# Performance work log

Hardware: AMD Instinct MI355X
Metric: run time of the kernel (lower is better)

The kernel has to match this reference:

```python
import jax, jax.numpy as jnp
import numpy as np

B, C, D, H, W = 4, 128, 16, 16, 16
CQ = C // 8

def setup_inputs() -> dict:
    key = jax.random.key(0)
    ks = jax.random.split(key, 8)
    s = 0.05
    return {
        "x": jax.random.normal(ks[0], (B, C, D, H, W), dtype=jnp.float32),
        "wq": jax.random.normal(ks[1], (CQ, C), dtype=jnp.float32) * s,
        "bq": jax.random.normal(ks[2], (CQ,), dtype=jnp.float32) * s,
        "wk": jax.random.normal(ks[3], (CQ, C), dtype=jnp.float32) * s,
        "bk": jax.random.normal(ks[4], (CQ,), dtype=jnp.float32) * s,
        "wv": jax.random.normal(ks[5], (C, C), dtype=jnp.float32) * s,
        "bv": jax.random.normal(ks[6], (C,), dtype=jnp.float32) * s,
        "gamma": jax.random.normal(ks[7], (1,), dtype=jnp.float32),
    }

def reference(x, wq, bq, wk, bk, wv, bv, gamma):
    b, c, d, h, w = x.shape
    n = d * h * w
    xf = x.reshape(b, c, n)                                  # [B,C,N]
    # 1x1x1 convs == channel-wise linear projections
    q = jnp.einsum('bcn,qc->bqn', xf, wq) + bq[None, :, None]  # [B,CQ,N]
    k = jnp.einsum('bcn,qc->bqn', xf, wk) + bk[None, :, None]  # [B,CQ,N]
    v = jnp.einsum('bcn,oc->bon', xf, wv) + bv[None, :, None]  # [B,C,N]
    # energy[b,i,j] = sum_c q[b,c,i] * k[b,c,j]  (query permuted to [B,N,CQ])
    energy = jnp.einsum('bci,bcj->bij', q, k)                # [B,N,N]
    attn = jax.nn.softmax(energy, axis=-1)                   # [B,N,N]
    # out = bmm(value, attn^T): out[b,c,i] = sum_j v[b,c,j] * attn[b,i,j]
    out = jnp.einsum('bcj,bij->bci', v, attn)                # [B,C,N]
    out = out.reshape(b, c, d, h, w)
    return gamma[0] * out + x
```

## Files before the change

### kernel.cpp

```cpp
#include <hip/hip_runtime.h>
#include <stdint.h>

#define NT 4096
#define L2E 1.44269504f

typedef short s16x8 __attribute__((ext_vector_type(8)));
typedef short s16x4 __attribute__((ext_vector_type(4)));
typedef float f32x16 __attribute__((ext_vector_type(16)));
typedef float f32x4 __attribute__((ext_vector_type(4)));

__device__ __forceinline__ unsigned short f2bf(float f) {
  unsigned int u = __float_as_uint(f);
  u = u + 0x7FFFu + ((u >> 16) & 1u);
  return (unsigned short)(u >> 16);
}

__device__ __forceinline__ void pack_pa(const float* p, s16x8* pa) {
  unsigned w8[8];
#pragma unroll
  for (int m = 0; m < 8; ++m)
    asm("v_cvt_pk_bf16_f32 %0, %1, %2" : "=v"(w8[m]) : "v"(p[2 * m]), "v"(p[2 * m + 1]));
  unsigned a0 = w8[0], b0 = w8[2]; asm("v_permlane32_swap_b32 %0, %1" : "+v"(a0), "+v"(b0));
  unsigned a1 = w8[1], b1 = w8[3]; asm("v_permlane32_swap_b32 %0, %1" : "+v"(a1), "+v"(b1));
  unsigned c0 = w8[4], d0 = w8[6]; asm("v_permlane32_swap_b32 %0, %1" : "+v"(c0), "+v"(d0));
  unsigned c1 = w8[5], d1 = w8[7]; asm("v_permlane32_swap_b32 %0, %1" : "+v"(c1), "+v"(d1));
  union PW { unsigned u[4]; s16x8 v; } q0, q1;
  q0.u[0] = a0; q0.u[1] = a1; q0.u[2] = b0; q0.u[3] = b1;
  q1.u[0] = c0; q1.u[1] = c1; q1.u[2] = d0; q1.u[3] = d1;
  pa[0] = q0.v; pa[1] = q1.v;
}

__device__ __forceinline__ void merge_write(float* scr, const f32x16 (&acc)[2][4],
                                            int lc, int hi) {
#pragma unroll
  for (int isub = 0; isub < 2; ++isub)
#pragma unroll
    for (int cb = 0; cb < 4; ++cb)
#pragma unroll
      for (int r = 0; r < 16; ++r) {
        int i = isub * 32 + (r & 3) + 8 * (r >> 2) + 4 * hi;
        scr[i * 132 + cb * 32 + lc] = acc[isub][cb][r];
      }
}
__device__ __forceinline__ void merge_add(const float* scr, f32x16 (&acc)[2][4],
                                          int lc, int hi) {
#pragma unroll
  for (int isub = 0; isub < 2; ++isub)
#pragma unroll
    for (int cb = 0; cb < 4; ++cb)
#pragma unroll
      for (int r = 0; r < 16; ++r) {
        int i = isub * 32 + (r & 3) + 8 * (r >> 2) + 4 * hi;
        acc[isub][cb][r] += scr[i * 132 + cb * 32 + lc];
      }
}

__global__ __launch_bounds__(512, 2) void proj_kern(
    const float* __restrict__ x,
    const float* __restrict__ wq, const float* __restrict__ bq,
    const float* __restrict__ wk, const float* __restrict__ bk,
    const float* __restrict__ wv, const float* __restrict__ bv,
    short* __restrict__ qws, short* __restrict__ kws, short* __restrict__ vfrag) {
  __shared__ __align__(16) unsigned short w_s[160 * 128];
  __shared__ __align__(16) unsigned short xv_s[128 * 72];

  int t = threadIdx.x;
  int blk = blockIdx.x;
  int b = blk >> 6;
  int n0 = (blk & 63) * 64;

  for (int i4 = t; i4 < 5120; i4 += 512) {
    int row = i4 >> 5, ka = (i4 & 31) * 4;
    f32x4 v;
    float sc = 1.0f;
    if (row < 128)      v = *(const f32x4*)(wv + row * 128 + ka);
    else if (row < 144) v = *(const f32x4*)(wq + (row - 128) * 128 + ka);
    else              { v = *(const f32x4*)(wk + (row - 144) * 128 + ka); sc = L2E; }
    s16x4 o;
#pragma unroll
    for (int j = 0; j < 4; ++j) o[j] = (short)f2bf(v[j] * sc);
    unsigned byt = ((unsigned)(ka * 2)) ^ (((unsigned)row & 7u) << 4);
    *(s16x4*)((char*)w_s + row * 256 + byt) = o;
  }
  {
    int cL = t >> 4, nn4 = (t & 15) * 4;
    for (int cc = 0; cc < 128; cc += 32) {
      int c = cc + cL;
      f32x4 v = *(const f32x4*)(x + ((size_t)b * 128 + c) * NT + n0 + nn4);
      s16x4 o;
#pragma unroll
      for (int j = 0; j < 4; ++j) o[j] = (short)f2bf(v[j]);
      *(s16x4*)(xv_s + c * 64 + nn4) = o;
    }
  }
  __syncthreads();

  int w = t >> 6, lane = t & 63, lc = lane & 31, hi = lane >> 5;
  int rblk = w >> 1, nc = w & 1;
  int nn = nc * 32 + lc;

  f32x16 zf = {0.f,0.f,0.f,0.f,0.f,0.f,0.f,0.f,0.f,0.f,0.f,0.f,0.f,0.f,0.f,0.f};
  f32x16 acc = zf, acc2 = zf;

#pragma unroll
  for (int kk = 0; kk < 8; ++kk) {
    int kb0 = kk * 16 + hi * 8;
    s16x8 xf;
#pragma unroll
    for (int e = 0; e < 8; ++e) xf[e] = (short)xv_s[(kb0 + e) * 64 + nn];
    unsigned byt = ((unsigned)(kk * 32 + hi * 16)) ^ (((unsigned)lc & 7u) << 4);
    s16x8 af = *(const s16x8*)((const char*)w_s + (rblk * 32 + lc) * 256 + byt);
    acc = __builtin_amdgcn_mfma_f32_32x32x16_bf16(af, xf, acc, 0, 0, 0);
    if (rblk == 3) {
      s16x8 af2 = *(const s16x8*)((const char*)w_s + (128 + lc) * 256 + byt);
      acc2 = __builtin_amdgcn_mfma_f32_32x32x16_bf16(af2, xf, acc2, 0, 0, 0);
    }
  }

  if (rblk == 3) {
    size_t nidx = ((size_t)b * NT + n0 + nn) * 16;
    s16x4 q0, q1, k0, k1;
#pragma unroll
    for (int j = 0; j < 4; ++j) {
      q0[j] = (short)f2bf(acc2[j]      + bq[j + 4 * hi]);
      q1[j] = (short)f2bf(acc2[j + 4]  + bq[j + 8 + 4 * hi]);
      k0[j] = (short)f2bf(acc2[j + 8]  + bk[j + 4 * hi] * L2E);
      k1[j] = (short)f2bf(acc2[j + 12] + bk[j + 8 + 4 * hi] * L2E);
    }
    *(s16x4*)(qws + nidx + 4 * hi)     = q0;
    *(s16x4*)(qws + nidx + 8 + 4 * hi) = q1;
    *(s16x4*)(kws + nidx + 4 * hi)     = k0;
    *(s16x4*)(kws + nidx + 8 + 4 * hi) = k1;
  }

  __syncthreads();
#pragma unroll
  for (int r = 0; r < 16; ++r) {
    int c = rblk * 32 + (r & 3) + 8 * (r >> 2) + 4 * hi;
    xv_s[c * 72 + nn] = f2bf(acc[r] + bv[c]);
  }
  __syncthreads();
#pragma unroll
  for (int p = 0; p < 2; ++p) {
    int gid = t + p * 512;
    int c = gid & 127, ng = gid >> 7;
    s16x8 v = *(const s16x8*)(xv_s + c * 72 + ng * 8);
    size_t idx = (((size_t)b * 256 + (n0 >> 4) + (ng >> 1)) * 128 + c) * 16 + (ng & 1) * 8;
    *(s16x8*)(vfrag + idx) = v;
  }
}

__global__ __launch_bounds__(512, 2) void attn_mfma(
    const short* __restrict__ qws, const short* __restrict__ kws, const short* __restrict__ vfrag,
    const float* __restrict__ x, const float* __restrict__ gp, float* __restrict__ out) {
  __shared__ __align__(16) unsigned char lds[69888];

  int g = blockIdx.x;
  int gg = (g & 7) * 32 + (g >> 3);
  int b = gg >> 6;
  int it = gg & 63;
  int t = threadIdx.x;
  int w = t >> 6, lane = t & 63, lc = lane & 31, hi = lane >> 5;
  int jt0 = w * 512;

  const short* qb = qws + (size_t)b * NT * 16;
  const short* kb = kws + (size_t)b * NT * 16;
  const short* vfb = vfrag + (size_t)b * 256 * 128 * 16;

  s16x8 qf0 = *(const s16x8*)(qb + (size_t)(it * 64 + lc) * 16 + hi * 8);
  s16x8 qf1 = *(const s16x8*)(qb + (size_t)(it * 64 + 32 + lc) * 16 + hi * 8);

  f32x16 zf = {0.f,0.f,0.f,0.f,0.f,0.f,0.f,0.f,0.f,0.f,0.f,0.f,0.f,0.f,0.f,0.f};
  f32x16 acc[2][4];
#pragma unroll
  for (int i = 0; i < 2; ++i)
#pragma unroll
    for (int j = 0; j < 4; ++j) acc[i][j] = zf;
  float lsum0 = 0.f, lsum1 = 0.f;

  s16x8 kf = *(const s16x8*)(kb + (size_t)(jt0 + lc) * 16 + hi * 8);

  for (int st = 0; st < 16; ++st) {
    int jtb = (jt0 >> 4) + st * 2;
    s16x8 vB[2][4];
#pragma unroll
    for (int sl = 0; sl < 2; ++sl)
#pragma unroll
      for (int cb = 0; cb < 4; ++cb)
        vB[sl][cb] = *(const s16x8*)(vfb + ((size_t)(jtb + sl) * 128 + cb * 32 + lc) * 16 + hi * 8);
    s16x8 kn = kf;
    if (st < 15)
      kn = *(const s16x8*)(kb + (size_t)(jt0 + (st + 1) * 32 + lc) * 16 + hi * 8);

    f32x16 e0 = __builtin_amdgcn_mfma_f32_32x32x16_bf16(kf, qf0, zf, 0, 0, 0);
    f32x16 e1 = __builtin_amdgcn_mfma_f32_32x32x16_bf16(kf, qf1, zf, 0, 0, 0);

    float p0[16], p1[16];
#pragma unroll
    for (int r = 0; r < 16; ++r) { p0[r] = __builtin_amdgcn_exp2f(e0[r]); p1[r] = __builtin_amdgcn_exp2f(e1[r]); }
    float a0 = 0.f, a1 = 0.f;
#pragma unroll
    for (int r = 0; r < 16; ++r) { a0 += p0[r]; a1 += p1[r]; }
    lsum0 += a0; lsum1 += a1;

    s16x8 pa0[2], pa1[2];
    pack_pa(p0, pa0);
    pack_pa(p1, pa1);

#pragma unroll
    for (int sl = 0; sl < 2; ++sl)
#pragma unroll
      for (int cb = 0; cb < 4; ++cb) {
        acc[0][cb] = __builtin_amdgcn_mfma_f32_32x32x16_bf16(pa0[sl], vB[sl][cb], acc[0][cb], 0, 0, 0);
        acc[1][cb] = __builtin_amdgcn_mfma_f32_32x32x16_bf16(pa1[sl], vB[sl][cb], acc[1][cb], 0, 0, 0);
      }
    kf = kn;
  }

  float* rg0  = (float*)lds;
  float* rg1  = (float*)(lds + 33792);
  float* lsc  = (float*)(lds + 67584);
  float* linv = (float*)(lds + 69632);

  float lf0 = lsum0 + __shfl_xor(lsum0, 32);
  float lf1 = lsum1 + __shfl_xor(lsum1, 32);
  if (hi == 0) { lsc[w * 64 + lc] = lf0; lsc[w * 64 + 32 + lc] = lf1; }
  __syncthreads();
  if (t < 64) {
    float L = 0.f;
#pragma unroll
    for (int w2 = 0; w2 < 8; ++w2) L += lsc[w2 * 64 + t];
    linv[t] = 1.0f / L;
  }
  if (w == 4) merge_write(rg0, acc, lc, hi);
  if (w == 5) merge_write(rg1, acc, lc, hi);
  __syncthreads();
  if (w == 0) merge_add(rg0, acc, lc, hi);
  if (w == 1) merge_add(rg1, acc, lc, hi);
  __syncthreads();
  if (w == 6) merge_write(rg0, acc, lc, hi);
  if (w == 7) merge_write(rg1, acc, lc, hi);
  __syncthreads();
  if (w == 2) merge_add(rg0, acc, lc, hi);
  if (w == 3) merge_add(rg1, acc, lc, hi);
  __syncthreads();
  if (w == 2) merge_write(rg0, acc, lc, hi);
  if (w == 3) merge_write(rg1, acc, lc, hi);
  __syncthreads();
  if (w == 0) merge_add(rg0, acc, lc, hi);
  if (w == 1) merge_add(rg1, acc, lc, hi);
  __syncthreads();
  if (w == 1) merge_write(rg0, acc, lc, hi);
  __syncthreads();
  if (w == 0) {
    merge_add(rg0, acc, lc, hi);
    merge_write(rg0, acc, lc, hi);
  }
  __syncthreads();

  float gam = gp[0];
  int cc = t >> 2, iq = t & 3;
  const float* xb = x + ((size_t)b * 128 + cc) * NT + it * 64 + iq * 16;
  float* ob = out + ((size_t)b * 128 + cc) * NT + it * 64 + iq * 16;
#pragma unroll
  for (int q2 = 0; q2 < 4; ++q2) {
    f32x4 xv = *(const f32x4*)(xb + q2 * 4);
    f32x4 ov;
#pragma unroll
    for (int j = 0; j < 4; ++j) {
      int i = iq * 16 + q2 * 4 + j;
      ov[j] = gam * rg0[i * 132 + cc] * linv[i] + xv[j];
    }
    *(f32x4*)(ob + q2 * 4) = ov;
  }
}

extern "C" void kernel_launch(void* const* d_in, const int* in_sizes, int n_in,
                              void* d_out, int out_size, void* d_ws, size_t ws_size,
                              hipStream_t stream) {
  const float* x     = (const float*)d_in[0];
  const float* wq    = (const float*)d_in[1];
  const float* bq    = (const float*)d_in[2];
  const float* wk    = (const float*)d_in[3];
  const float* bk    = (const float*)d_in[4];
  const float* wv    = (const float*)d_in[5];
  const float* bv    = (const float*)d_in[6];
  const float* gamma = (const float*)d_in[7];
  float* out = (float*)d_out;

  short* qws   = (short*)d_ws;
  short* kws   = qws + (size_t)4 * NT * 16;
  short* vfrag = kws + (size_t)4 * NT * 16;

  proj_kern<<<256, 512, 0, stream>>>(x, wq, bq, wk, bk, wv, bv, qws, kws, vfrag);
  attn_mfma<<<256, 512, 0, stream>>>(qws, kws, vfrag, x, gamma, out);
}
```

Baseline: 43.54 us.

## Shrink attention tile to 32 queries over 4 waves with 512 blocks

The attention kernel now handles 32 query rows per block with 4 waves of 256 threads, each wave covering 1024 keys, and launches 512 blocks instead of 256 blocks of 512 threads. The smaller accumulator set and LDS footprint are meant to raise occupancy and shorten the cross-wave merge. V loads are split into two halves interleaved with MFMA groups wrapped in setprio. The cost is that each K/V fragment is reused by only one query tile, which doubles K/V traffic relative to the amount of compute.

```diff
diff --git a/kernel.cpp b/kernel.cpp
--- a/kernel.cpp
+++ b/kernel.cpp
@@ -30,29 +30,25 @@
   pa[0] = q0.v; pa[1] = q1.v;
 }
 
-__device__ __forceinline__ void merge_write(float* scr, const f32x16 (&acc)[2][4],
+__device__ __forceinline__ void merge_write(float* scr, const f32x16 (&acc)[4],
                                             int lc, int hi) {
 #pragma unroll
-  for (int isub = 0; isub < 2; ++isub)
-#pragma unroll
-    for (int cb = 0; cb < 4; ++cb)
-#pragma unroll
-      for (int r = 0; r < 16; ++r) {
-        int i = isub * 32 + (r & 3) + 8 * (r >> 2) + 4 * hi;
-        scr[i * 132 + cb * 32 + lc] = acc[isub][cb][r];
-      }
-}
-__device__ __forceinline__ void merge_add(const float* scr, f32x16 (&acc)[2][4],
+  for (int cb = 0; cb < 4; ++cb)
+#pragma unroll
+    for (int r = 0; r < 16; ++r) {
+      int i = (r & 3) + 8 * (r >> 2) + 4 * hi;
+      scr[i * 132 + cb * 32 + lc] = acc[cb][r];
+    }
+}
+__device__ __forceinline__ void merge_add(const float* scr, f32x16 (&acc)[4],
                                           int lc, int hi) {
 #pragma unroll
-  for (int isub = 0; isub < 2; ++isub)
-#pragma unroll
-    for (int cb = 0; cb < 4; ++cb)
-#pragma unroll
-      for (int r = 0; r < 16; ++r) {
-        int i = isub * 32 + (r & 3) + 8 * (r >> 2) + 4 * hi;
-        acc[isub][cb][r] += scr[i * 132 + cb * 32 + lc];
-      }
+  for (int cb = 0; cb < 4; ++cb)
+#pragma unroll
+    for (int r = 0; r < 16; ++r) {
+      int i = (r & 3) + 8 * (r >> 2) + 4 * hi;
+      acc[cb][r] += scr[i * 132 + cb * 32 + lc];
+    }
 }
 
 __global__ __launch_bounds__(512, 2) void proj_kern(
@@ -150,103 +146,83 @@
   }
 }
 
-__global__ __launch_bounds__(512, 2) void attn_mfma(
+__global__ __launch_bounds__(256, 4) void attn_mfma(
     const short* __restrict__ qws, const short* __restrict__ kws, const short* __restrict__ vfrag,
     const float* __restrict__ x, const float* __restrict__ gp, float* __restrict__ out) {
-  __shared__ __align__(16) unsigned char lds[69888];
+  __shared__ __align__(16) unsigned char lds[34432];
 
   int g = blockIdx.x;
-  int gg = (g & 7) * 32 + (g >> 3);
-  int b = gg >> 6;
-  int it = gg & 63;
+  int gg = (g & 7) * 64 + (g >> 3);
+  int b = gg >> 7;
+  int it = gg & 127;
   int t = threadIdx.x;
   int w = t >> 6, lane = t & 63, lc = lane & 31, hi = lane >> 5;
-  int jt0 = w * 512;
+  int jt0 = w * 1024;
 
   const short* qb = qws + (size_t)b * NT * 16;
   const short* kb = kws + (size_t)b * NT * 16;
   const short* vfb = vfrag + (size_t)b * 256 * 128 * 16;
 
-  s16x8 qf0 = *(const s16x8*)(qb + (size_t)(it * 64 + lc) * 16 + hi * 8);
-  s16x8 qf1 = *(const s16x8*)(qb + (size_t)(it * 64 + 32 + lc) * 16 + hi * 8);
+  s16x8 qf = *(const s16x8*)(qb + (size_t)(it * 32 + lc) * 16 + hi * 8);
 
   f32x16 zf = {0.f,0.f,0.f,0.f,0.f,0.f,0.f,0.f,0.f,0.f,0.f,0.f,0.f,0.f,0.f,0.f};
-  f32x16 acc[2][4];
-#pragma unroll
-  for (int i = 0; i < 2; ++i)
-#pragma unroll
-    for (int j = 0; j < 4; ++j) acc[i][j] = zf;
-  float lsum0 = 0.f, lsum1 = 0.f;
-
-  s16x8 kf = *(const s16x8*)(kb + (size_t)(jt0 + lc) * 16 + hi * 8);
-
-  for (int st = 0; st < 16; ++st) {
-    int jtb = (jt0 >> 4) + st * 2;
-    s16x8 vB[2][4];
-#pragma unroll
-    for (int sl = 0; sl < 2; ++sl)
-#pragma unroll
-      for (int cb = 0; cb < 4; ++cb)
-        vB[sl][cb] = *(const s16x8*)(vfb + ((size_t)(jtb + sl) * 128 + cb * 32 + lc) * 16 + hi * 8);
-    s16x8 kn = kf;
-    if (st < 15)
-      kn = *(const s16x8*)(kb + (size_t)(jt0 + (st + 1) * 32 + lc) * 16 + hi * 8);
-
-    f32x16 e0 = __builtin_amdgcn_mfma_f32_32x32x16_bf16(kf, qf0, zf, 0, 0, 0);
-    f32x16 e1 = __builtin_amdgcn_mfma_f32_32x32x16_bf16(kf, qf1, zf, 0, 0, 0);
-
-    float p0[16], p1[16];
-#pragma unroll
-    for (int r = 0; r < 16; ++r) { p0[r] = __builtin_amdgcn_exp2f(e0[r]); p1[r] = __builtin_amdgcn_exp2f(e1[r]); }
-    float a0 = 0.f, a1 = 0.f;
-#pragma unroll
-    for (int r = 0; r < 16; ++r) { a0 += p0[r]; a1 += p1[r]; }
-    lsum0 += a0; lsum1 += a1;
-
-    s16x8 pa0[2], pa1[2];
-    pack_pa(p0, pa0);
-    pack_pa(p1, pa1);
-
-#pragma unroll
-    for (int sl = 0; sl < 2; ++sl)
-#pragma unroll
-      for (int cb = 0; cb < 4; ++cb) {
-        acc[0][cb] = __builtin_amdgcn_mfma_f32_32x32x16_bf16(pa0[sl], vB[sl][cb], acc[0][cb], 0, 0, 0);
-        acc[1][cb] = __builtin_amdgcn_mfma_f32_32x32x16_bf16(pa1[sl], vB[sl][cb], acc[1][cb], 0, 0, 0);
-      }
-    kf = kn;
+  f32x16 acc[4];
+#pragma unroll
+  for (int j = 0; j < 4; ++j) acc[j] = zf;
+  float lsum = 0.f;
+
+  for (int st = 0; st < 32; ++st) {
+    int j0 = jt0 + st * 32;
+    int jtb = j0 >> 4;
+    s16x8 kf = *(const s16x8*)(kb + (size_t)(j0 + lc) * 16 + hi * 8);
+    s16x8 v0[4];
+#pragma unroll
+    for (int cb = 0; cb < 4; ++cb)
+      v0[cb] = *(const s16x8*)(vfb + ((size_t)jtb * 128 + cb * 32 + lc) * 16 + hi * 8);
+
+    f32x16 e = __builtin_amdgcn_mfma_f32_32x32x16_bf16(kf, qf, zf, 0, 0, 0);
+#pragma unroll
+    for (int r = 0; r < 16; ++r) e[r] = __builtin_amdgcn_exp2f(e[r]);
+    float a0 = 0.f;
+#pragma unroll
+    for (int r = 0; r < 16; ++r) a0 += e[r];
+    lsum += a0;
+
+    s16x8 pa[2];
+    pack_pa((const float*)&e, pa);
+
+    __builtin_amdgcn_s_setprio(1);
+#pragma unroll
+    for (int cb = 0; cb < 4; ++cb)
+      acc[cb] = __builtin_amdgcn_mfma_f32_32x32x16_bf16(pa[0], v0[cb], acc[cb], 0, 0, 0);
+    __builtin_amdgcn_s_setprio(0);
+
+    s16x8 v1[4];
+#pragma unroll
+    for (int cb = 0; cb < 4; ++cb)
+      v1[cb] = *(const s16x8*)(vfb + ((size_t)(jtb + 1) * 128 + cb * 32 + lc) * 16 + hi * 8);
+
+    __builtin_amdgcn_s_setprio(1);
+#pragma unroll
+    for (int cb = 0; cb < 4; ++cb)
+      acc[cb] = __builtin_amdgcn_mfma_f32_32x32x16_bf16(pa[1], v1[cb], acc[cb], 0, 0, 0);
+    __builtin_amdgcn_s_setprio(0);
   }
 
   float* rg0  = (float*)lds;
-  float* rg1  = (float*)(lds + 33792);
-  float* lsc  = (float*)(lds + 67584);
-  float* linv = (float*)(lds + 69632);
-
-  float lf0 = lsum0 + __shfl_xor(lsum0, 32);
-  float lf1 = lsum1 + __shfl_xor(lsum1, 32);
-  if (hi == 0) { lsc[w * 64 + lc] = lf0; lsc[w * 64 + 32 + lc] = lf1; }
-  __syncthreads();
-  if (t < 64) {
-    float L = 0.f;
-#pragma unroll
-    for (int w2 = 0; w2 < 8; ++w2) L += lsc[w2 * 64 + t];
-    linv[t] = 1.0f / L;
-  }
-  if (w == 4) merge_write(rg0, acc, lc, hi);
-  if (w == 5) merge_write(rg1, acc, lc, hi);
-  __syncthreads();
-  if (w == 0) merge_add(rg0, acc, lc, hi);
-  if (w == 1) merge_add(rg1, acc, lc, hi);
-  __syncthreads();
-  if (w == 6) merge_write(rg0, acc, lc, hi);
-  if (w == 7) merge_write(rg1, acc, lc, hi);
-  __syncthreads();
-  if (w == 2) merge_add(rg0, acc, lc, hi);
-  if (w == 3) merge_add(rg1, acc, lc, hi);
-  __syncthreads();
+  float* rg1  = (float*)(lds + 16896);
+  float* lsc  = (float*)(lds + 33792);
+  float* linv = (float*)(lds + 34304);
+
+  float lf = lsum + __shfl_xor(lsum, 32);
+  if (hi == 0) lsc[w * 32 + lc] = lf;
   if (w == 2) merge_write(rg0, acc, lc, hi);
   if (w == 3) merge_write(rg1, acc, lc, hi);
   __syncthreads();
+  if (t < 32) {
+    float L = lsc[t] + lsc[32 + t] + lsc[64 + t] + lsc[96 + t];
+    linv[t] = 1.0f / L;
+  }
   if (w == 0) merge_add(rg0, acc, lc, hi);
   if (w == 1) merge_add(rg1, acc, lc, hi);
   __syncthreads();
@@ -259,16 +235,16 @@
   __syncthreads();
 
   float gam = gp[0];
-  int cc = t >> 2, iq = t & 3;
-  const float* xb = x + ((size_t)b * 128 + cc) * NT + it * 64 + iq * 16;
-  float* ob = out + ((size_t)b * 128 + cc) * NT + it * 64 + iq * 16;
+  int cc = t >> 1, ih = (t & 1) * 16;
+  const float* xb = x + ((size_t)b * 128 + cc) * NT + it * 32 + ih;
+  float* ob = out + ((size_t)b * 128 + cc) * NT + it * 32 + ih;
 #pragma unroll
   for (int q2 = 0; q2 < 4; ++q2) {
     f32x4 xv = *(const f32x4*)(xb + q2 * 4);
     f32x4 ov;
 #pragma unroll
     for (int j = 0; j < 4; ++j) {
-      int i = iq * 16 + q2 * 4 + j;
+      int i = ih + q2 * 4 + j;
       ov[j] = gam * rg0[i * 132 + cc] * linv[i] + xv[j];
     }
     *(f32x4*)(ob + q2 * 4) = ov;
@@ -293,5 +269,5 @@
   short* vfrag = kws + (size_t)4 * NT * 16;
 
   proj_kern<<<256, 512, 0, stream>>>(x, wq, bq, wk, bk, wv, bv, qws, kws, vfrag);
-  attn_mfma<<<256, 512, 0, stream>>>(qws, kws, vfrag, x, gamma, out);
-}
+  attn_mfma<<<512, 256, 0, stream>>>(qws, kws, vfrag, x, gamma, out);
+}
```

Measured after the change: 45.05 us. 3.5% more time.

## Split waves into producer/consumer pairs passing softmax tiles through LDS ring

Applied to the files above, without the earlier changes.

Each pair of waves now shares a 1024-key range: the even wave computes QK^T scores, exp2, and bf16 packing and writes the P tiles into a double-buffered LDS ring. The odd wave loads V fragments and runs the PV MFMAs from that ring, so the exp/pack VALU work can overlap the PV matrix work. Only four accumulating waves remain, which shortens the cross-wave reduction tree. In exchange, every step needs a block-wide barrier, and the P tiles make an extra round trip through LDS.

```diff
diff --git a/kernel.cpp b/kernel.cpp
--- a/kernel.cpp
+++ b/kernel.cpp
@@ -153,7 +153,7 @@
 __global__ __launch_bounds__(512, 2) void attn_mfma(
     const short* __restrict__ qws, const short* __restrict__ kws, const short* __restrict__ vfrag,
     const float* __restrict__ x, const float* __restrict__ gp, float* __restrict__ out) {
-  __shared__ __align__(16) unsigned char lds[69888];
+  __shared__ __align__(16) unsigned char lds[68864];
 
   int g = blockIdx.x;
   int gg = (g & 7) * 32 + (g >> 3);
@@ -161,14 +161,14 @@
   int it = gg & 63;
   int t = threadIdx.x;
   int w = t >> 6, lane = t & 63, lc = lane & 31, hi = lane >> 5;
-  int jt0 = w * 512;
+  int pair = w >> 1, role = w & 1;
+  int jt0 = pair * 1024;
 
   const short* qb = qws + (size_t)b * NT * 16;
   const short* kb = kws + (size_t)b * NT * 16;
   const short* vfb = vfrag + (size_t)b * 256 * 128 * 16;
 
-  s16x8 qf0 = *(const s16x8*)(qb + (size_t)(it * 64 + lc) * 16 + hi * 8);
-  s16x8 qf1 = *(const s16x8*)(qb + (size_t)(it * 64 + 32 + lc) * 16 + hi * 8);
+  unsigned char* ring = lds + pair * 8192;
 
   f32x16 zf = {0.f,0.f,0.f,0.f,0.f,0.f,0.f,0.f,0.f,0.f,0.f,0.f,0.f,0.f,0.f,0.f};
   f32x16 acc[2][4];
@@ -178,84 +178,123 @@
     for (int j = 0; j < 4; ++j) acc[i][j] = zf;
   float lsum0 = 0.f, lsum1 = 0.f;
 
-  s16x8 kf = *(const s16x8*)(kb + (size_t)(jt0 + lc) * 16 + hi * 8);
-
-  for (int st = 0; st < 16; ++st) {
-    int jtb = (jt0 >> 4) + st * 2;
-    s16x8 vB[2][4];
+  if (role == 0) {
+    s16x8 qf0 = *(const s16x8*)(qb + (size_t)(it * 64 + lc) * 16 + hi * 8);
+    s16x8 qf1 = *(const s16x8*)(qb + (size_t)(it * 64 + 32 + lc) * 16 + hi * 8);
+    s16x8 kfC = *(const s16x8*)(kb + (size_t)(jt0 + lc) * 16 + hi * 8);
+    for (int st = 0; st < 32; ++st) {
+      s16x8 kfN = kfC;
+      if (st < 31)
+        kfN = *(const s16x8*)(kb + (size_t)(jt0 + (st + 1) * 32 + lc) * 16 + hi * 8);
+
+      f32x16 e0 = __builtin_amdgcn_mfma_f32_32x32x16_bf16(kfC, qf0, zf, 0, 0, 0);
+      f32x16 e1 = __builtin_amdgcn_mfma_f32_32x32x16_bf16(kfC, qf1, zf, 0, 0, 0);
+#pragma unroll
+      for (int r = 0; r < 16; ++r) e0[r] = __builtin_amdgcn_exp2f(e0[r]);
+#pragma unroll
+      for (int r = 0; r < 16; ++r) e1[r] = __builtin_amdgcn_exp2f(e1[r]);
+      float a0 = 0.f, a1 = 0.f;
+#pragma unroll
+      for (int r = 0; r < 16; ++r) { a0 += e0[r]; a1 += e1[r]; }
+      lsum0 += a0; lsum1 += a1;
+
+      s16x8 pa0[2], pa1[2];
+      pack_pa((const float*)&e0, pa0);
+      pack_pa((const float*)&e1, pa1);
+
+      unsigned char* slot = ring + (st & 1) * 4096 + lane * 16;
+      *(s16x8*)(slot)        = pa0[0];
+      *(s16x8*)(slot + 1024) = pa0[1];
+      *(s16x8*)(slot + 2048) = pa1[0];
+      *(s16x8*)(slot + 3072) = pa1[1];
+      kfC = kfN;
+      __syncthreads();
+    }
+    __syncthreads();
+  } else {
+    s16x8 vA[2][4], vB[2][4];
 #pragma unroll
     for (int sl = 0; sl < 2; ++sl)
 #pragma unroll
       for (int cb = 0; cb < 4; ++cb)
-        vB[sl][cb] = *(const s16x8*)(vfb + ((size_t)(jtb + sl) * 128 + cb * 32 + lc) * 16 + hi * 8);
-    s16x8 kn = kf;
-    if (st < 15)
-      kn = *(const s16x8*)(kb + (size_t)(jt0 + (st + 1) * 32 + lc) * 16 + hi * 8);
-
-    f32x16 e0 = __builtin_amdgcn_mfma_f32_32x32x16_bf16(kf, qf0, zf, 0, 0, 0);
-    f32x16 e1 = __builtin_amdgcn_mfma_f32_32x32x16_bf16(kf, qf1, zf, 0, 0, 0);
-
-    float p0[16], p1[16];
-#pragma unroll
-    for (int r = 0; r < 16; ++r) { p0[r] = __builtin_amdgcn_exp2f(e0[r]); p1[r] = __builtin_amdgcn_exp2f(e1[r]); }
-    float a0 = 0.f, a1 = 0.f;
-#pragma unroll
-    for (int r = 0; r < 16; ++r) { a0 += p0[r]; a1 += p1[r]; }
-    lsum0 += a0; lsum1 += a1;
-
-    s16x8 pa0[2], pa1[2];
-    pack_pa(p0, pa0);
-    pack_pa(p1, pa1);
-
-#pragma unroll
-    for (int sl = 0; sl < 2; ++sl)
-#pragma unroll
-      for (int cb = 0; cb < 4; ++cb) {
-        acc[0][cb] = __builtin_amdgcn_mfma_f32_32x32x16_bf16(pa0[sl], vB[sl][cb], acc[0][cb], 0, 0, 0);
-        acc[1][cb] = __builtin_amdgcn_mfma_f32_32x32x16_bf16(pa1[sl], vB[sl][cb], acc[1][cb], 0, 0, 0);
-      }
-    kf = kn;
+        vA[sl][cb] = *(const s16x8*)(vfb + ((size_t)((jt0 >> 4) + sl) * 128 + cb * 32 + lc) * 16 + hi * 8);
+    __syncthreads();
+
+    for (int kk = 0; kk < 16; ++kk) {
+      int st = 2 * kk;
+      if (st + 1 < 32) {
+        int jtb = (jt0 >> 4) + (st + 1) * 2;
+#pragma unroll
+        for (int sl = 0; sl < 2; ++sl)
+#pragma unroll
+          for (int cb = 0; cb < 4; ++cb)
+            vB[sl][cb] = *(const s16x8*)(vfb + ((size_t)(jtb + sl) * 128 + cb * 32 + lc) * 16 + hi * 8);
+      }
+      {
+        const unsigned char* slot = ring + lane * 16;
+        s16x8 pa0[2], pa1[2];
+        pa0[0] = *(const s16x8*)(slot);
+        pa0[1] = *(const s16x8*)(slot + 1024);
+        pa1[0] = *(const s16x8*)(slot + 2048);
+        pa1[1] = *(const s16x8*)(slot + 3072);
+#pragma unroll
+        for (int sl = 0; sl < 2; ++sl)
+#pragma unroll
+          for (int cb = 0; cb < 4; ++cb) {
+            acc[0][cb] = __builtin_amdgcn_mfma_f32_32x32x16_bf16(pa0[sl], vA[sl][cb], acc[0][cb], 0, 0, 0);
+            acc[1][cb] = __builtin_amdgcn_mfma_f32_32x32x16_bf16(pa1[sl], vA[sl][cb], acc[1][cb], 0, 0, 0);
+          }
+      }
+      __syncthreads();
+
+      if (st + 2 < 32) {
+        int jtb = (jt0 >> 4) + (st + 2) * 2;
+#pragma unroll
+        for (int sl = 0; sl < 2; ++sl)
+#pragma unroll
+          for (int cb = 0; cb < 4; ++cb)
+            vA[sl][cb] = *(const s16x8*)(vfb + ((size_t)(jtb + sl) * 128 + cb * 32 + lc) * 16 + hi * 8);
+      }
+      {
+        const unsigned char* slot = ring + 4096 + lane * 16;
+        s16x8 pa0[2], pa1[2];
+        pa0[0] = *(const s16x8*)(slot);
+        pa0[1] = *(const s16x8*)(slot + 1024);
+        pa1[0] = *(const s16x8*)(slot + 2048);
+        pa1[1] = *(const s16x8*)(slot + 3072);
+#pragma unroll
+        for (int sl = 0; sl < 2; ++sl)
+#pragma unroll
+          for (int cb = 0; cb < 4; ++cb) {
+            acc[0][cb] = __builtin_amdgcn_mfma_f32_32x32x16_bf16(pa0[sl], vB[sl][cb], acc[0][cb], 0, 0, 0);
+            acc[1][cb] = __builtin_amdgcn_mfma_f32_32x32x16_bf16(pa1[sl], vB[sl][cb], acc[1][cb], 0, 0, 0);
+          }
+      }
+      __syncthreads();
+    }
   }
 
   float* rg0  = (float*)lds;
   float* rg1  = (float*)(lds + 33792);
   float* lsc  = (float*)(lds + 67584);
-  float* linv = (float*)(lds + 69632);
+  float* linv = (float*)(lds + 68608);
 
   float lf0 = lsum0 + __shfl_xor(lsum0, 32);
   float lf1 = lsum1 + __shfl_xor(lsum1, 32);
-  if (hi == 0) { lsc[w * 64 + lc] = lf0; lsc[w * 64 + 32 + lc] = lf1; }
+  if (role == 0 && hi == 0) { lsc[pair * 64 + lc] = lf0; lsc[pair * 64 + 32 + lc] = lf1; }
+  if (w == 3) merge_write(rg0, acc, lc, hi);
+  if (w == 7) merge_write(rg1, acc, lc, hi);
   __syncthreads();
   if (t < 64) {
-    float L = 0.f;
-#pragma unroll
-    for (int w2 = 0; w2 < 8; ++w2) L += lsc[w2 * 64 + t];
+    float L = lsc[t] + lsc[64 + t] + lsc[128 + t] + lsc[192 + t];
     linv[t] = 1.0f / L;
   }
-  if (w == 4) merge_write(rg0, acc, lc, hi);
+  if (w == 1) merge_add(rg0, acc, lc, hi);
+  if (w == 5) merge_add(rg1, acc, lc, hi);
+  __syncthreads();
   if (w == 5) merge_write(rg1, acc, lc, hi);
   __syncthreads();
-  if (w == 0) merge_add(rg0, acc, lc, hi);
-  if (w == 1) merge_add(rg1, acc, lc, hi);
-  __syncthreads();
-  if (w == 6) merge_write(rg0, acc, lc, hi);
-  if (w == 7) merge_write(rg1, acc, lc, hi);
-  __syncthreads();
-  if (w == 2) merge_add(rg0, acc, lc, hi);
-  if (w == 3) merge_add(rg1, acc, lc, hi);
-  __syncthreads();
-  if (w == 2) merge_write(rg0, acc, lc, hi);
-  if (w == 3) merge_write(rg1, acc, lc, hi);
-  __syncthreads();
-  if (w == 0) merge_add(rg0, acc, lc, hi);
-  if (w == 1) merge_add(rg1, acc, lc, hi);
-  __syncthreads();
-  if (w == 1) merge_write(rg0, acc, lc, hi);
-  __syncthreads();
-  if (w == 0) {
-    merge_add(rg0, acc, lc, hi);
-    merge_write(rg0, acc, lc, hi);
-  }
+  if (w == 1) { merge_add(rg1, acc, lc, hi); merge_write(rg0, acc, lc, hi); }
   __syncthreads();
 
   float gam = gp[0];
```

After: 43.68 us. No clear change (+0.3%).
